# Performance work log

Measured on AMD Instinct MI355X. Metric: run time of the kernel, lower is better.

## Reference

```python
import jax, jax.numpy as jnp
import numpy as np

B, T = 256, 4096
L = 128          # shapelet_length
K = 128          # num_shapelets
K_TOP = 5


def setup_inputs() -> dict:
    key = jax.random.key(0)
    kx, ks = jax.random.split(key)
    x = jax.random.normal(kx, (B, T), dtype=jnp.float32)
    shapelets = jax.random.normal(ks, (K, L), dtype=jnp.float32) * 0.1
    return {"x": x, "shapelets": shapelets}


def reference(x, shapelets):
    # x: [B, T], shapelets: [K, L]
    N = x.shape[1] - L + 1  # number of sliding windows
    # Gather overlapping windows: x_win [B, N, L]
    idx = jnp.arange(N)[:, None] + jnp.arange(L)[None, :]
    x_win = x[:, idx]
    # Per-window mean removal
    x_norm = x_win - jnp.mean(x_win, axis=2, keepdims=True)
    # Per-shapelet mean removal
    s_norm = shapelets - jnp.mean(shapelets, axis=1, keepdims=True)
    # Correlation: [B, N, K]
    corr = jnp.einsum('bnl,kl->bnk', x_norm, s_norm)
    k_val = min(K_TOP, N)
    # top-k over window dim N -> move N to last axis
    topk_vals, _ = jax.lax.top_k(jnp.transpose(corr, (0, 2, 1)), k_val)  # [B, K, k]
    p1 = topk_vals[:, :, 0]
    p2 = topk_vals[:, :, 1] if k_val >= 2 else p1
    p_mean = jnp.mean(topk_vals, axis=2)
    dominance = jax.nn.relu(p1 - p2)
    return jnp.concatenate([p1, p_mean, p2, dominance], axis=1)  # [B, 4K]
```

## Files before the change

### kernel.cpp

```cpp
#include <hip/hip_runtime.h>

#define T_LEN 4096
#define N_WIN 3969
#define K_SH  128
#define L_SH  128
#define B_SZ  256
#define NT    31

#define SSTR  136
#define XSTR  4360

#define NEG_INF (-3.402823466e38f)

typedef __attribute__((ext_vector_type(8))) __bf16 bf16x8;
typedef __attribute__((ext_vector_type(4))) float f32x4;
typedef _Float16 h2 __attribute__((ext_vector_type(2)));

__device__ __forceinline__ unsigned short f2bf(float f) {
    union { float f; unsigned int u; } c; c.f = f;
    unsigned int u = c.u + 0x7fff + ((c.u >> 16) & 1u);
    return (unsigned short)(u >> 16);
}
__device__ __forceinline__ unsigned int pack2(unsigned short lo, unsigned short hi) {
    return (unsigned int)lo | ((unsigned int)hi << 16);
}

__device__ __forceinline__ h2 max2(h2 a, h2 b) { return __builtin_elementwise_max(a, b); }
__device__ __forceinline__ h2 min2(h2 a, h2 b) { return __builtin_elementwise_min(a, b); }
__device__ __forceinline__ h2 cvt2(float lo, float hi) {
    return __builtin_bit_cast(h2, __builtin_amdgcn_cvt_pkrtz(lo, hi));
}
__device__ __forceinline__ void ce2(h2& hi, h2& lo) {
    const h2 m = max2(hi, lo);
    lo = min2(hi, lo);
    hi = m;
}
__device__ __forceinline__ void sort4_2(h2& a, h2& b, h2& c, h2& d) {
    ce2(a, b); ce2(c, d); ce2(a, c); ce2(b, d); ce2(b, c);
}
__device__ __forceinline__ void merge44_top5_2(h2 a0, h2 a1, h2 a2, h2 a3,
                                               h2 b0, h2 b1, h2 b2, h2 b3,
                                               h2& r0, h2& r1, h2& r2, h2& r3, h2& r4) {
    ce2(a0, b0); ce2(a2, b2); ce2(b0, a2);
    ce2(a1, b1); ce2(a3, b3); ce2(b1, a3);
    r0 = a0;
    r1 = a1; r2 = b0; ce2(r1, r2);
    r3 = b1; r4 = a2; ce2(r3, r4);
}
__device__ __forceinline__ void merge55_2(h2& r0, h2& r1, h2& r2, h2& r3, h2& r4,
                                          h2 s0, h2 s1, h2 s2, h2 s3, h2 s4) {
    const h2 m00 = min2(r0, s0);
    const h2 m10 = min2(r1, s0), m01 = min2(r0, s1);
    const h2 m20 = min2(r2, s0), m11 = min2(r1, s1), m02 = min2(r0, s2);
    const h2 m30 = min2(r3, s0), m21 = min2(r2, s1), m12 = min2(r1, s2), m03 = min2(r0, s3);
    const h2 n0 = max2(r0, s0);
    const h2 n1 = max2(max2(r1, s1), m00);
    const h2 n2 = max2(max2(r2, s2), max2(m10, m01));
    const h2 n3 = max2(max2(max2(r3, s3), m20), max2(m11, m02));
    const h2 n4 = max2(max2(max2(r4, s4), max2(m30, m03)), max2(m21, m12));
    r0 = n0; r1 = n1; r2 = n2; r3 = n3; r4 = n4;
}
__device__ __forceinline__ void insert1_2(h2 v, h2* rt) {
    h2 b = max2(rt[4], v); h2 m;
    m = max2(rt[3], b);     b     = min2(rt[3], b);     rt[3] = m;
    m = max2(rt[2], rt[3]); rt[3] = min2(rt[2], rt[3]); rt[2] = m;
    m = max2(rt[1], rt[2]); rt[2] = min2(rt[1], rt[2]); rt[1] = m;
    m = max2(rt[0], rt[1]); rt[1] = min2(rt[0], rt[1]); rt[0] = m;
    rt[4] = b;
}
__device__ __forceinline__ void select32(const f32x4* acc0, const f32x4* acc1, h2* rt) {
    h2 p[16];
    #pragma unroll
    for (int m = 0; m < 4; ++m)
        #pragma unroll
        for (int i = 0; i < 4; ++i)
            p[4 * m + i] = cvt2(acc0[m][i], acc1[m][i]);
    sort4_2(p[0], p[1], p[2],  p[3]);
    sort4_2(p[4], p[5], p[6],  p[7]);
    sort4_2(p[8], p[9], p[10], p[11]);
    sort4_2(p[12], p[13], p[14], p[15]);
    h2 u0, u1, u2, u3, u4, v0, v1, v2, v3, v4;
    merge44_top5_2(p[0], p[1], p[2],  p[3],  p[4],  p[5],  p[6],  p[7],  u0, u1, u2, u3, u4);
    merge44_top5_2(p[8], p[9], p[10], p[11], p[12], p[13], p[14], p[15], v0, v1, v2, v3, v4);
    merge55_2(u0, u1, u2, u3, u4, v0, v1, v2, v3, v4);
    merge55_2(rt[0], rt[1], rt[2], rt[3], rt[4], u0, u1, u2, u3, u4);
}

__global__ __launch_bounds__(512, 1)
void shapelet_fused_kernel(const float* __restrict__ x,
                           const float* __restrict__ s,
                           float* __restrict__ out) {
    __shared__ __align__(16) unsigned short ldsS[K_SH * SSTR];
    __shared__ __align__(16) unsigned short ldsX[8 * XSTR];

    const int t    = threadIdx.x;
    const int lane = t & 63;
    const int w    = t >> 6;
    const int r    = lane & 15;
    const int q    = lane >> 4;
    const int c7   = lane & 7;
    const int ub   = (lane >> 3) & 1;
    const int mh   = w >> 2;
    const int wp   = w & 3;
    const int mtb  = 4 * mh;
    const int b    = blockIdx.x;

    {
        const int k = t >> 2, qd = t & 3;
        const float4* srow = (const float4*)(s + k * L_SH + qd * 32);
        float4 v[8];
        float sum = 0.0f;
        #pragma unroll
        for (int j = 0; j < 8; ++j) {
            v[j] = srow[j];
            sum += (v[j].x + v[j].y) + (v[j].z + v[j].w);
        }
        sum += __shfl_xor(sum, 1);
        sum += __shfl_xor(sum, 2);
        const float mean = sum * (1.0f / 128.0f);
        uint4* dst = (uint4*)((char*)ldsS + k * (SSTR * 2) + qd * 64);
        #pragma unroll
        for (int j = 0; j < 4; ++j) {
            uint4 o;
            o.x = pack2(f2bf(v[2*j].x - mean),   f2bf(v[2*j].y - mean));
            o.y = pack2(f2bf(v[2*j].z - mean),   f2bf(v[2*j].w - mean));
            o.z = pack2(f2bf(v[2*j+1].x - mean), f2bf(v[2*j+1].y - mean));
            o.w = pack2(f2bf(v[2*j+1].z - mean), f2bf(v[2*j+1].w - mean));
            dst[j] = o;
        }
        if (qd == 3) *(uint4*)((char*)ldsS + k * (SSTR * 2) + 256) = make_uint4(0,0,0,0);
    }

    {
        const float* __restrict__ xb = x + (size_t)b * T_LEN;
        const int a = t & 7;
        for (int i = (t >> 3); i < XSTR / 8; i += 64) {
            const int p0 = 8 * i;
            float xv[16];
            if (p0 + 16 <= T_LEN) {
                const float4* sp = (const float4*)(xb + p0);
                #pragma unroll
                for (int j = 0; j < 4; ++j) *(float4*)(xv + 4 * j) = sp[j];
            } else {
                #pragma unroll
                for (int j = 0; j < 16; ++j) {
                    const int gi = p0 + j;
                    xv[j] = (gi < T_LEN) ? xb[gi] : 0.0f;
                }
            }
            unsigned short bv[16];
            #pragma unroll
            for (int j = 0; j < 16; ++j) bv[j] = f2bf(xv[j]);
            uint4 o;
            o.x = pack2(bv[a],     bv[a + 1]);
            o.y = pack2(bv[a + 2], bv[a + 3]);
            o.z = pack2(bv[a + 4], bv[a + 5]);
            o.w = pack2(bv[a + 6], bv[a + 7]);
            *(uint4*)((char*)ldsX + a * (XSTR * 2) + 2 * p0) = o;
        }
    }
    __syncthreads();

    bf16x8 bfr[2][4];
    #pragma unroll
    for (int kk = 0; kk < 2; ++kk)
        #pragma unroll
        for (int c = 0; c < 4; ++c)
            bfr[kk][c] = __builtin_bit_cast(bf16x8, *(const uint4*)(
                (const char*)ldsS + ((2 * wp + kk) * 16 + r) * (SSTR * 2) + 64 * c + 16 * q));

    h2 rt[5];
    #pragma unroll
    for (int i = 0; i < 5; ++i) rt[i] = __builtin_bit_cast(h2, 0xFC00FC00u);

    const char* xp = (const char*)ldsX + c7 * (XSTR * 2) + 16 * q + 16 * ub + 32 * mtb;

    bf16x8 afrA[10], afrB[10];
    #pragma unroll
    for (int j = 0; j < 10; ++j)
        afrA[j] = __builtin_bit_cast(bf16x8, *(const uint4*)(xp + 32 * j));

    int off = 256;

#define TILE_STEP(CUR, NXT)                                                     \
    {                                                                           \
        f32x4 acc0[4], acc1[4];                                                 \
        _Pragma("unroll")                                                       \
        for (int m = 0; m < 4; ++m) {                                           \
            acc0[m] = (f32x4){0.f, 0.f, 0.f, 0.f};                              \
            acc1[m] = (f32x4){0.f, 0.f, 0.f, 0.f};                              \
        }                                                                       \
        _Pragma("unroll")                                                       \
        for (int c = 0; c < 4; ++c) {                                           \
            _Pragma("unroll")                                                   \
            for (int m = 0; m < 4; ++m) {                                       \
                acc0[m] = __builtin_amdgcn_mfma_f32_16x16x32_bf16(CUR[m + 2*c], bfr[0][c], acc0[m], 0, 0, 0); \
                acc1[m] = __builtin_amdgcn_mfma_f32_16x16x32_bf16(CUR[m + 2*c], bfr[1][c], acc1[m], 0, 0, 0); \
            }                                                                   \
        }                                                                       \
        _Pragma("unroll")                                                       \
        for (int j = 0; j < 10; ++j)                                            \
            NXT[j] = __builtin_bit_cast(bf16x8, *(const uint4*)(xp + off + 32 * j)); \
        off += 256;                                                             \
        select32(acc0, acc1, rt);                                               \
    }

    for (int tt = 0; tt < 15; ++tt) {
        TILE_STEP(afrA, afrB)
        TILE_STEP(afrB, afrA)
    }
    TILE_STEP(afrA, afrB)
#undef TILE_STEP

    if (mh == 0) {
        f32x4 e0 = (f32x4){0.f, 0.f, 0.f, 0.f};
        f32x4 e1 = (f32x4){0.f, 0.f, 0.f, 0.f};
        const char* eb = (const char*)ldsX + c7 * (XSTR * 2) + 7936 + 16 * q + 16 * ub;
        #pragma unroll
        for (int c = 0; c < 4; ++c) {
            const bf16x8 af = __builtin_bit_cast(bf16x8, *(const uint4*)(eb + 64 * c));
            e0 = __builtin_amdgcn_mfma_f32_16x16x32_bf16(af, bfr[0][c], e0, 0, 0, 0);
            e1 = __builtin_amdgcn_mfma_f32_16x16x32_bf16(af, bfr[1][c], e1, 0, 0, 0);
        }
        if (q == 0) insert1_2(cvt2(e0[0], e1[0]), rt);
    }

    #pragma unroll
    for (int mask = 16; mask <= 32; mask <<= 1) {
        h2 s[5];
        #pragma unroll
        for (int i = 0; i < 5; ++i)
            s[i] = __builtin_bit_cast(h2, __shfl_xor(__builtin_bit_cast(int, rt[i]), mask));
        merge55_2(rt[0], rt[1], rt[2], rt[3], rt[4], s[0], s[1], s[2], s[3], s[4]);
    }

    __syncthreads();
    unsigned int* pbuf = (unsigned int*)ldsS;
    if (mh == 1 && q == 0) {
        unsigned int* p = pbuf + (wp * 16 + r) * 5;
        #pragma unroll
        for (int i = 0; i < 5; ++i) p[i] = __builtin_bit_cast(unsigned int, rt[i]);
    }
    __syncthreads();
    if (mh == 0 && q == 0) {
        const unsigned int* p = pbuf + (wp * 16 + r) * 5;
        h2 s[5];
        #pragma unroll
        for (int i = 0; i < 5; ++i) s[i] = __builtin_bit_cast(h2, p[i]);
        merge55_2(rt[0], rt[1], rt[2], rt[3], rt[4], s[0], s[1], s[2], s[3], s[4]);

        const float A0 = (float)rt[0][0], A1 = (float)rt[1][0], A2 = (float)rt[2][0],
                    A3 = (float)rt[3][0], A4 = (float)rt[4][0];
        const float B0 = (float)rt[0][1], B1 = (float)rt[1][1], B2 = (float)rt[2][1],
                    B3 = (float)rt[3][1], B4 = (float)rt[4][1];
        float* ob = out + (size_t)b * (4 * K_SH);
        const int ksA = 32 * wp + r, ksB = ksA + 16;
        const float mA = (((A0 + A1) + (A2 + A3)) + A4) * 0.2f;
        const float mB = (((B0 + B1) + (B2 + B3)) + B4) * 0.2f;
        ob[ksA]           = A0;
        ob[K_SH + ksA]    = mA;
        ob[2*K_SH + ksA]  = A1;
        ob[3*K_SH + ksA]  = fmaxf(A0 - A1, 0.0f);
        ob[ksB]           = B0;
        ob[K_SH + ksB]    = mB;
        ob[2*K_SH + ksB]  = B1;
        ob[3*K_SH + ksB]  = fmaxf(B0 - B1, 0.0f);
    }
}

extern "C" void kernel_launch(void* const* d_in, const int* in_sizes, int n_in,
                              void* d_out, int out_size, void* d_ws, size_t ws_size,
                              hipStream_t stream) {
    const float* x = (const float*)d_in[0];
    const float* s = (const float*)d_in[1];
    float* out = (float*)d_out;
    shapelet_fused_kernel<<<B_SZ, 512, 0, stream>>>(x, s, out);
}
```

Baseline: 96.61 us.

## Double block to 1024 threads, splitting window tiles between two wave groups

The block grows to 16 waves, split into two groups that take alternating 256-byte window tiles. The extra group's partial top-5 lists are merged through LDS in a three-way final reduction. The register double-buffer prefetch of A fragments is dropped in favour of loading each tile's fragments at the start of its step, relying on more resident waves to hide LDS latency. This risks register pressure under a 1024-thread launch bound and loses explicit prefetch.

```diff
diff --git a/kernel.cpp b/kernel.cpp
--- a/kernel.cpp
+++ b/kernel.cpp
@@ -5,12 +5,9 @@
 #define K_SH  128
 #define L_SH  128
 #define B_SZ  256
-#define NT    31
 
 #define SSTR  136
 #define XSTR  4360
-
-#define NEG_INF (-3.402823466e38f)
 
 typedef __attribute__((ext_vector_type(8))) __bf16 bf16x8;
 typedef __attribute__((ext_vector_type(4))) float f32x4;
@@ -86,7 +83,7 @@
     merge55_2(rt[0], rt[1], rt[2], rt[3], rt[4], u0, u1, u2, u3, u4);
 }
 
-__global__ __launch_bounds__(512, 1)
+__global__ __launch_bounds__(1024)
 void shapelet_fused_kernel(const float* __restrict__ x,
                            const float* __restrict__ s,
                            float* __restrict__ out) {
@@ -100,27 +97,30 @@
     const int q    = lane >> 4;
     const int c7   = lane & 7;
     const int ub   = (lane >> 3) & 1;
-    const int mh   = w >> 2;
-    const int wp   = w & 3;
+    const int g    = w >> 3;
+    const int w7   = w & 7;
+    const int mh   = w7 >> 2;
+    const int wp   = w7 & 3;
     const int mtb  = 4 * mh;
     const int b    = blockIdx.x;
 
     {
-        const int k = t >> 2, qd = t & 3;
-        const float4* srow = (const float4*)(s + k * L_SH + qd * 32);
-        float4 v[8];
+        const int k = t >> 3, e8 = t & 7;
+        const float4* srow = (const float4*)(s + k * L_SH + e8 * 16);
+        float4 v[4];
         float sum = 0.0f;
         #pragma unroll
-        for (int j = 0; j < 8; ++j) {
+        for (int j = 0; j < 4; ++j) {
             v[j] = srow[j];
             sum += (v[j].x + v[j].y) + (v[j].z + v[j].w);
         }
         sum += __shfl_xor(sum, 1);
         sum += __shfl_xor(sum, 2);
+        sum += __shfl_xor(sum, 4);
         const float mean = sum * (1.0f / 128.0f);
-        uint4* dst = (uint4*)((char*)ldsS + k * (SSTR * 2) + qd * 64);
-        #pragma unroll
-        for (int j = 0; j < 4; ++j) {
+        uint4* dst = (uint4*)((char*)ldsS + k * (SSTR * 2) + e8 * 32);
+        #pragma unroll
+        for (int j = 0; j < 2; ++j) {
             uint4 o;
             o.x = pack2(f2bf(v[2*j].x - mean),   f2bf(v[2*j].y - mean));
             o.y = pack2(f2bf(v[2*j].z - mean),   f2bf(v[2*j].w - mean));
@@ -128,13 +128,13 @@
             o.w = pack2(f2bf(v[2*j+1].z - mean), f2bf(v[2*j+1].w - mean));
             dst[j] = o;
         }
-        if (qd == 3) *(uint4*)((char*)ldsS + k * (SSTR * 2) + 256) = make_uint4(0,0,0,0);
+        if (e8 == 7) *(uint4*)((char*)ldsS + k * (SSTR * 2) + 256) = make_uint4(0,0,0,0);
     }
 
     {
         const float* __restrict__ xb = x + (size_t)b * T_LEN;
         const int a = t & 7;
-        for (int i = (t >> 3); i < XSTR / 8; i += 64) {
+        for (int i = (t >> 3); i < XSTR / 8; i += 128) {
             const int p0 = 8 * i;
             float xv[16];
             if (p0 + 16 <= T_LEN) {
@@ -173,17 +173,16 @@
     #pragma unroll
     for (int i = 0; i < 5; ++i) rt[i] = __builtin_bit_cast(h2, 0xFC00FC00u);
 
-    const char* xp = (const char*)ldsX + c7 * (XSTR * 2) + 16 * q + 16 * ub + 32 * mtb;
-
-    bf16x8 afrA[10], afrB[10];
-    #pragma unroll
-    for (int j = 0; j < 10; ++j)
-        afrA[j] = __builtin_bit_cast(bf16x8, *(const uint4*)(xp + 32 * j));
-
-    int off = 256;
-
-#define TILE_STEP(CUR, NXT)                                                     \
+    const char* xp = (const char*)ldsX + c7 * (XSTR * 2) + 16 * q + 16 * ub + 32 * mtb
+                   + g * 256;
+
+#define TILE_STEP                                                               \
     {                                                                           \
+        bf16x8 afr[10];                                                         \
+        _Pragma("unroll")                                                       \
+        for (int j = 0; j < 10; ++j)                                            \
+            afr[j] = __builtin_bit_cast(bf16x8, *(const uint4*)(xp + 32 * j));  \
+        xp += 512;                                                              \
         f32x4 acc0[4], acc1[4];                                                 \
         _Pragma("unroll")                                                       \
         for (int m = 0; m < 4; ++m) {                                           \
@@ -194,25 +193,18 @@
         for (int c = 0; c < 4; ++c) {                                           \
             _Pragma("unroll")                                                   \
             for (int m = 0; m < 4; ++m) {                                       \
-                acc0[m] = __builtin_amdgcn_mfma_f32_16x16x32_bf16(CUR[m + 2*c], bfr[0][c], acc0[m], 0, 0, 0); \
-                acc1[m] = __builtin_amdgcn_mfma_f32_16x16x32_bf16(CUR[m + 2*c], bfr[1][c], acc1[m], 0, 0, 0); \
+                acc0[m] = __builtin_amdgcn_mfma_f32_16x16x32_bf16(afr[m + 2*c], bfr[0][c], acc0[m], 0, 0, 0); \
+                acc1[m] = __builtin_amdgcn_mfma_f32_16x16x32_bf16(afr[m + 2*c], bfr[1][c], acc1[m], 0, 0, 0); \
             }                                                                   \
         }                                                                       \
-        _Pragma("unroll")                                                       \
-        for (int j = 0; j < 10; ++j)                                            \
-            NXT[j] = __builtin_bit_cast(bf16x8, *(const uint4*)(xp + off + 32 * j)); \
-        off += 256;                                                             \
         select32(acc0, acc1, rt);                                               \
     }
 
-    for (int tt = 0; tt < 15; ++tt) {
-        TILE_STEP(afrA, afrB)
-        TILE_STEP(afrB, afrA)
-    }
-    TILE_STEP(afrA, afrB)
+    for (int st = 0; st < 15; ++st) { TILE_STEP }
+    if (g == 0) { TILE_STEP }
 #undef TILE_STEP
 
-    if (mh == 0) {
+    if (g == 1 && mh == 0) {
         f32x4 e0 = (f32x4){0.f, 0.f, 0.f, 0.f};
         f32x4 e1 = (f32x4){0.f, 0.f, 0.f, 0.f};
         const char* eb = (const char*)ldsX + c7 * (XSTR * 2) + 7936 + 16 * q + 16 * ub;
@@ -227,27 +219,31 @@
 
     #pragma unroll
     for (int mask = 16; mask <= 32; mask <<= 1) {
-        h2 s[5];
+        h2 sv[5];
         #pragma unroll
         for (int i = 0; i < 5; ++i)
-            s[i] = __builtin_bit_cast(h2, __shfl_xor(__builtin_bit_cast(int, rt[i]), mask));
-        merge55_2(rt[0], rt[1], rt[2], rt[3], rt[4], s[0], s[1], s[2], s[3], s[4]);
+            sv[i] = __builtin_bit_cast(h2, __shfl_xor(__builtin_bit_cast(int, rt[i]), mask));
+        merge55_2(rt[0], rt[1], rt[2], rt[3], rt[4], sv[0], sv[1], sv[2], sv[3], sv[4]);
     }
 
     __syncthreads();
     unsigned int* pbuf = (unsigned int*)ldsS;
-    if (mh == 1 && q == 0) {
-        unsigned int* p = pbuf + (wp * 16 + r) * 5;
+    if ((g != 0 || mh != 0) && q == 0) {
+        const int reg = (g * 2 + mh) - 1;
+        unsigned int* p = pbuf + ((reg * 64) + wp * 16 + r) * 5;
         #pragma unroll
         for (int i = 0; i < 5; ++i) p[i] = __builtin_bit_cast(unsigned int, rt[i]);
     }
     __syncthreads();
-    if (mh == 0 && q == 0) {
-        const unsigned int* p = pbuf + (wp * 16 + r) * 5;
-        h2 s[5];
-        #pragma unroll
-        for (int i = 0; i < 5; ++i) s[i] = __builtin_bit_cast(h2, p[i]);
-        merge55_2(rt[0], rt[1], rt[2], rt[3], rt[4], s[0], s[1], s[2], s[3], s[4]);
+    if (g == 0 && mh == 0 && q == 0) {
+        #pragma unroll
+        for (int reg = 0; reg < 3; ++reg) {
+            const unsigned int* p = pbuf + ((reg * 64) + wp * 16 + r) * 5;
+            h2 sv[5];
+            #pragma unroll
+            for (int i = 0; i < 5; ++i) sv[i] = __builtin_bit_cast(h2, p[i]);
+            merge55_2(rt[0], rt[1], rt[2], rt[3], rt[4], sv[0], sv[1], sv[2], sv[3], sv[4]);
+        }
 
         const float A0 = (float)rt[0][0], A1 = (float)rt[1][0], A2 = (float)rt[2][0],
                     A3 = (float)rt[3][0], A4 = (float)rt[4][0];
@@ -274,5 +270,5 @@
     const float* x = (const float*)d_in[0];
     const float* s = (const float*)d_in[1];
     float* out = (float*)d_out;
-    shapelet_fused_kernel<<<B_SZ, 512, 0, stream>>>(x, s, out);
-}
+    shapelet_fused_kernel<<<B_SZ, 1024, 0, stream>>>(x, s, out);
+}
```

New measurement: 94.70 us. 2.0% less time.
